# Performance work log

Hardware: AMD Instinct MI355X
Metric: run time of the kernel (lower is better)

The kernel has to match this reference:

```python
import jax, jax.numpy as jnp
import numpy as np

N = 8192
IN_F = 512
OUT_F = 64
ALPHA = 0.2  # LeakyReLU negative slope
NEG_INF = -9e15


def setup_inputs() -> dict:
    key = jax.random.key(0)
    k1, k2, k3, k4 = jax.random.split(key, 4)
    x = jax.random.normal(k1, (N, IN_F), dtype=jnp.float32)
    adj = jax.random.randint(k2, (N, N), 0, 2, dtype=jnp.int32)
    # xavier_uniform with gain=1.414
    def xavier(k, shape, gain=1.414):
        fan_in, fan_out = shape[0], shape[1]
        a = gain * np.sqrt(6.0 / (fan_in + fan_out))
        return jax.random.uniform(k, shape, jnp.float32, -a, a)
    W = xavier(k3, (IN_F, OUT_F))
    a = xavier(k4, (2 * OUT_F, 1))
    return {"x": x, "adj": adj, "W": W, "a": a}


def reference(x, adj, W, a):
    h = x @ W  # [N, F]
    f = W.shape[1]
    # e[i,j] = leakyrelu([h_i, h_j] @ a) = leakyrelu(h_i@a1 + h_j@a2)
    e1 = h @ a[:f, 0]   # [N]
    e2 = h @ a[f:, 0]   # [N]
    e = jax.nn.leaky_relu(e1[:, None] + e2[None, :], negative_slope=ALPHA)  # [N, N]
    scores = jnp.where(adj > 0, e, NEG_INF)
    attention = jax.nn.softmax(scores, axis=1)  # dropout p=0.0 -> identity
    h_prime = attention @ h  # [N, F]
    return jax.nn.elu(h_prime)  # concat=True
```

## Files before the change

### kernel.cpp

```cpp
#include <hip/hip_runtime.h>
#include <hip/hip_bf16.h>

#define NN 8192
#define KF 512
#define FF 64
#define GAT_ALPHA 0.2f
#define MSHIFT 20.0f
#define LOG2E 1.44269504f

#define JSPLIT 16
#define JW (NN / JSPLIT)
#define KSTEPS (JW / 32)

#define HTS 520

#define EXP2F(x) __builtin_amdgcn_exp2f(x)

typedef __attribute__((ext_vector_type(8))) __bf16 bf16x8;
typedef __attribute__((ext_vector_type(4))) float f32x4;

__device__ __forceinline__ unsigned pack_bf16_rne(float hi, float lo) {
    unsigned uh = __float_as_uint(hi);
    unsigned ul = __float_as_uint(lo);
    uh = uh + 0x7FFFu + ((uh >> 16) & 1u);
    ul = ul + 0x7FFFu + ((ul >> 16) & 1u);
    return (uh & 0xFFFF0000u) | (ul >> 16);
}

__global__ __launch_bounds__(256) void gat_linear(
    const float* __restrict__ x, const float* __restrict__ W,
    const float* __restrict__ av, __hip_bfloat16* __restrict__ ht,
    float* __restrict__ e1, float* __restrict__ e2)
{
    __shared__ float xs[32][33];
    __shared__ float Ws[32][64];
    __shared__ float ep[2][32][17];

    const int t  = threadIdx.x;
    const int fq = t & 15;
    const int rq = t >> 4;
    const int i0 = blockIdx.x * 32;

    const int kl = t & 31, r0 = t >> 5;
    const int fw = t & 63, kq = t >> 6;

    float acc[2][4] = {};

    for (int kt = 0; kt < KF; kt += 32) {
        #pragma unroll
        for (int m = 0; m < 4; ++m)
            xs[kl][r0 + 8 * m] = x[(size_t)(i0 + r0 + 8 * m) * KF + kt + kl];
        #pragma unroll
        for (int m = 0; m < 8; ++m)
            Ws[kq + 4 * m][fw] = W[(size_t)(kt + kq + 4 * m) * FF + fw];
        __syncthreads();
        #pragma unroll
        for (int kk = 0; kk < 32; ++kk) {
            float x0 = xs[kk][rq * 2];
            float x1 = xs[kk][rq * 2 + 1];
            f32x4 wv = *(const f32x4*)&Ws[kk][fq * 4];
            #pragma unroll
            for (int v = 0; v < 4; ++v) {
                acc[0][v] += x0 * wv[v];
                acc[1][v] += x1 * wv[v];
            }
        }
        __syncthreads();
    }

    #pragma unroll
    for (int v = 0; v < 4; ++v) {
        int f = fq * 4 + v;
        unsigned w = pack_bf16_rne(acc[1][v], acc[0][v]);
        *(unsigned*)&ht[(size_t)f * NN + i0 + rq * 2] = w;
    }

    f32x4 a1v = *(const f32x4*)&av[fq * 4];
    f32x4 a2v = *(const f32x4*)&av[64 + fq * 4];
    #pragma unroll
    for (int u = 0; u < 2; ++u) {
        float s1 = 0.f, s2 = 0.f;
        #pragma unroll
        for (int v = 0; v < 4; ++v) {
            s1 += acc[u][v] * a1v[v];
            s2 += acc[u][v] * a2v[v];
        }
        ep[0][rq * 2 + u][fq] = s1;
        ep[1][rq * 2 + u][fq] = s2;
    }
    __syncthreads();
    if (t < 32) {
        float s1 = 0.f, s2 = 0.f;
        #pragma unroll
        for (int q = 0; q < 16; ++q) { s1 += ep[0][t][q]; s2 += ep[1][t][q]; }
        e1[i0 + t] = s1 * LOG2E;
        e2[i0 + t] = s2 * LOG2E;
    }
}

__global__ __launch_bounds__(256) void gat_attn(
    const int* __restrict__ adj, const __hip_bfloat16* __restrict__ ht,
    const float* __restrict__ e1, const float* __restrict__ e2,
    float* __restrict__ accs, float* __restrict__ lsums)
{
    __shared__ __hip_bfloat16 hs[64 * HTS];
    __shared__ float e2s[JW];
    __shared__ unsigned char msk[KSTEPS * 4 * 68];

    const int t     = threadIdx.x;
    const int lane  = t & 63;
    const int wv    = t >> 6;
    const int n16   = lane & 15;
    const int quad  = lane >> 4;
    const int split = blockIdx.x & (JSPLIT - 1);
    const int i0b   = (blockIdx.x >> 4) * 64;
    const int i0    = i0b + wv * 16;
    const int j0    = split * JW;
    const int rowl  = wv * 16 + n16;
    const int row   = i0 + n16;

    #pragma unroll
    for (int k = 0; k < 16; ++k) {
        int g  = t + k * 256;
        int f  = g >> 6;
        int jl = (g & 63) * 8;
        *(bf16x8*)&hs[f * HTS + jl] =
            *(const bf16x8*)&ht[(size_t)f * NN + j0 + jl];
    }
    if (t < JW / 4)
        *(float4*)&e2s[t * 4] = *(const float4*)&e2[j0 + t * 4];

    {
        const int st = t & 15;
        #pragma unroll
        for (int rep = 0; rep < 4; ++rep) {
            const int r = rep * 16 + (t >> 4);
            const int* ap = adj + (size_t)(i0b + r) * NN + j0 + st * 32;
            unsigned w = 0;
            #pragma unroll
            for (int k = 0; k < 8; ++k) {
                int4 v = *(const int4*)(ap + k * 4);
                unsigned nib =  (unsigned)(v.x > 0)
                             | ((unsigned)(v.y > 0) << 1)
                             | ((unsigned)(v.z > 0) << 2)
                             | ((unsigned)(v.w > 0) << 3);
                w |= nib << (k * 4);
            }
            msk[(st * 4 + 0) * 68 + r] = (unsigned char)(w       & 0xFF);
            msk[(st * 4 + 1) * 68 + r] = (unsigned char)((w >> 8)  & 0xFF);
            msk[(st * 4 + 2) * 68 + r] = (unsigned char)((w >> 16) & 0xFF);
            msk[(st * 4 + 3) * 68 + r] = (unsigned char)((w >> 24) & 0xFF);
        }
    }
    __syncthreads();

    const float e1L = e1[row];
    float ms = e1L + MSHIFT * LOG2E;
    const float miL = ms > 0.f ? ms : GAT_ALPHA * ms;
    const float c0  = e1L - miL;
    const float c1  = GAT_ALPHA * e1L - miL;

    const __hip_bfloat16* hp = hs + rowl * 0 + n16 * HTS + quad * 8;
    const float* ep0 = e2s + quad * 8;

    f32x4 dacc0 = {0.f,0.f,0.f,0.f}, dacc1 = {0.f,0.f,0.f,0.f};
    f32x4 dacc2 = {0.f,0.f,0.f,0.f}, dacc3 = {0.f,0.f,0.f,0.f};
    f32x4 dl    = {0.f,0.f,0.f,0.f};

    typedef __attribute__((ext_vector_type(4))) int i32x4;
    const i32x4 ones_i = {0x3F803F80, 0x3F803F80, 0x3F803F80, 0x3F803F80};
    const bf16x8 ones  = __builtin_bit_cast(bf16x8, ones_i);

    unsigned mb = msk[(0 * 4 + quad) * 68 + rowl];
    f32x4  e0 = *(const f32x4*)(ep0);
    f32x4  ev = *(const f32x4*)(ep0 + 4);
    bf16x8 b0 = *(const bf16x8*)(hp);
    bf16x8 b1 = *(const bf16x8*)(hp + 16 * HTS);
    bf16x8 b2 = *(const bf16x8*)(hp + 32 * HTS);
    bf16x8 b3 = *(const bf16x8*)(hp + 48 * HTS);

    for (int st = 0; st < KSTEPS; ++st) {
        const unsigned mc = mb;
        const f32x4  ce0 = e0, cev = ev;
        const bf16x8 cb0 = b0, cb1 = b1, cb2 = b2, cb3 = b3;
        if (st + 1 < KSTEPS) {
            mb = msk[((st + 1) * 4 + quad) * 68 + rowl];
            e0 = *(const f32x4*)(ep0 + (st + 1) * 32);
            ev = *(const f32x4*)(ep0 + (st + 1) * 32 + 4);
            b0 = *(const bf16x8*)(hp + (st + 1) * 32);
            b1 = *(const bf16x8*)(hp + 16 * HTS + (st + 1) * 32);
            b2 = *(const bf16x8*)(hp + 32 * HTS + (st + 1) * 32);
            b3 = *(const bf16x8*)(hp + 48 * HTS + (st + 1) * 32);
        }

#define PJ(eval, bit)                                                          \
        ( ((mc >> (bit)) & 1u)                                                 \
            ? EXP2F(fmaxf(c0 + (eval), __builtin_fmaf(GAT_ALPHA, (eval), c1))) \
            : 0.f )
        float p0 = PJ(ce0.x, 0);
        float p1 = PJ(ce0.y, 1);
        float p2 = PJ(ce0.z, 2);
        float p3 = PJ(ce0.w, 3);
        float p4 = PJ(cev.x, 4);
        float p5 = PJ(cev.y, 5);
        float p6 = PJ(cev.z, 6);
        float p7 = PJ(cev.w, 7);
#undef PJ
        i32x4 iv;
        iv.x = (int)pack_bf16_rne(p1, p0);
        iv.y = (int)pack_bf16_rne(p3, p2);
        iv.z = (int)pack_bf16_rne(p5, p4);
        iv.w = (int)pack_bf16_rne(p7, p6);
        bf16x8 af = __builtin_bit_cast(bf16x8, iv);

        dacc0 = __builtin_amdgcn_mfma_f32_16x16x32_bf16(af, cb0, dacc0, 0, 0, 0);
        dacc1 = __builtin_amdgcn_mfma_f32_16x16x32_bf16(af, cb1, dacc1, 0, 0, 0);
        dacc2 = __builtin_amdgcn_mfma_f32_16x16x32_bf16(af, cb2, dacc2, 0, 0, 0);
        dacc3 = __builtin_amdgcn_mfma_f32_16x16x32_bf16(af, cb3, dacc3, 0, 0, 0);
        dl    = __builtin_amdgcn_mfma_f32_16x16x32_bf16(af, ones, dl, 0, 0, 0);
    }

    if (n16 == 0) {
        lsums[(size_t)split * NN + i0 + quad * 4 + 0] = dl.x;
        lsums[(size_t)split * NN + i0 + quad * 4 + 1] = dl.y;
        lsums[(size_t)split * NN + i0 + quad * 4 + 2] = dl.z;
        lsums[(size_t)split * NN + i0 + quad * 4 + 3] = dl.w;
    }

    float* ab = accs + (size_t)split * NN * FF + (size_t)(i0 + quad * 4) * FF + n16;
#define STORE4(dv, ftofs)                                                      \
    ab[0 * FF + (ftofs)] = (dv).x;                                             \
    ab[1 * FF + (ftofs)] = (dv).y;                                             \
    ab[2 * FF + (ftofs)] = (dv).z;                                             \
    ab[3 * FF + (ftofs)] = (dv).w;
    STORE4(dacc0, 0)
    STORE4(dacc1, 16)
    STORE4(dacc2, 32)
    STORE4(dacc3, 48)
#undef STORE4
}

__global__ __launch_bounds__(256) void gat_epilogue(
    const float* __restrict__ accs, const float* __restrict__ lsums,
    float* __restrict__ out)
{
    const int idx = (blockIdx.x * 256 + threadIdx.x) * 4;
    const int row = idx >> 6;

    float l = 0.f;
    #pragma unroll
    for (int s = 0; s < JSPLIT; ++s) l += lsums[(size_t)s * NN + row];

    f32x4 a = {0.f, 0.f, 0.f, 0.f};
    #pragma unroll
    for (int s = 0; s < JSPLIT; ++s) {
        f32x4 v = *(const f32x4*)(accs + (size_t)s * NN * FF + idx);
        a.x += v.x; a.y += v.y; a.z += v.z; a.w += v.w;
    }

    const float li = 1.f / l;
    f32x4 o;
    o.x = a.x * li; o.y = a.y * li; o.z = a.z * li; o.w = a.w * li;
    o.x = o.x > 0.f ? o.x : __expf(o.x) - 1.f;
    o.y = o.y > 0.f ? o.y : __expf(o.y) - 1.f;
    o.z = o.z > 0.f ? o.z : __expf(o.z) - 1.f;
    o.w = o.w > 0.f ? o.w : __expf(o.w) - 1.f;
    *(f32x4*)(out + idx) = o;
}

extern "C" void kernel_launch(void* const* d_in, const int* in_sizes, int n_in,
                              void* d_out, int out_size, void* d_ws, size_t ws_size,
                              hipStream_t stream) {
    const float* x   = (const float*)d_in[0];
    const int*   adj = (const int*)d_in[1];
    const float* W   = (const float*)d_in[2];
    const float* av  = (const float*)d_in[3];
    float* out = (float*)d_out;

    char* wsb = (char*)d_ws;
    __hip_bfloat16* ht = (__hip_bfloat16*)wsb;
    float* e1    = (float*)(wsb + (1 << 20));
    float* e2    = e1 + NN;
    float* accs  = e2 + NN;
    float* lsums = accs + (size_t)JSPLIT * NN * FF;

    gat_linear<<<256, 256, 0, stream>>>(x, W, av, ht, e1, e2);
    gat_attn<<<(NN / 64) * JSPLIT, 256, 0, stream>>>(adj, ht, e1, e2, accs, lsums);
    gat_epilogue<<<NN * FF / 1024, 256, 0, stream>>>(accs, lsums, out);
}
```

Baseline: 399.8 us.

## Stream adjacency and h directly from global memory, dropping LDS staging

Removes the shared-memory staging of the h tile, e2 slice and packed adjacency bitmask in the attention kernel. Each lane now reads its adjacency ints, e2 values and h fragments straight from global memory, with adjacency prefetched two steps ahead and the rest one step ahead. A minBlocks occupancy hint of 4 is added to launch_bounds. This drops the block-wide prologue and barrier and frees LDS to allow more resident blocks, but h and e2 reuse now depends on L2/L1 caching, and per-lane adjacency loads are less coalesced than the previous cooperative load.

```diff
diff --git a/kernel.cpp b/kernel.cpp
--- a/kernel.cpp
+++ b/kernel.cpp
@@ -12,12 +12,11 @@
 #define JW (NN / JSPLIT)
 #define KSTEPS (JW / 32)
 
-#define HTS 520
-
 #define EXP2F(x) __builtin_amdgcn_exp2f(x)
 
 typedef __attribute__((ext_vector_type(8))) __bf16 bf16x8;
 typedef __attribute__((ext_vector_type(4))) float f32x4;
+typedef __attribute__((ext_vector_type(4))) int i32x4;
 
 __device__ __forceinline__ unsigned pack_bf16_rne(float hi, float lo) {
     unsigned uh = __float_as_uint(hi);
@@ -98,61 +97,20 @@
     }
 }
 
-__global__ __launch_bounds__(256) void gat_attn(
+__global__ __launch_bounds__(256, 4) void gat_attn(
     const int* __restrict__ adj, const __hip_bfloat16* __restrict__ ht,
     const float* __restrict__ e1, const float* __restrict__ e2,
     float* __restrict__ accs, float* __restrict__ lsums)
 {
-    __shared__ __hip_bfloat16 hs[64 * HTS];
-    __shared__ float e2s[JW];
-    __shared__ unsigned char msk[KSTEPS * 4 * 68];
-
     const int t     = threadIdx.x;
     const int lane  = t & 63;
     const int wv    = t >> 6;
     const int n16   = lane & 15;
     const int quad  = lane >> 4;
     const int split = blockIdx.x & (JSPLIT - 1);
-    const int i0b   = (blockIdx.x >> 4) * 64;
-    const int i0    = i0b + wv * 16;
+    const int i0    = (blockIdx.x >> 4) * 64 + wv * 16;
     const int j0    = split * JW;
-    const int rowl  = wv * 16 + n16;
     const int row   = i0 + n16;
-
-    #pragma unroll
-    for (int k = 0; k < 16; ++k) {
-        int g  = t + k * 256;
-        int f  = g >> 6;
-        int jl = (g & 63) * 8;
-        *(bf16x8*)&hs[f * HTS + jl] =
-            *(const bf16x8*)&ht[(size_t)f * NN + j0 + jl];
-    }
-    if (t < JW / 4)
-        *(float4*)&e2s[t * 4] = *(const float4*)&e2[j0 + t * 4];
-
-    {
-        const int st = t & 15;
-        #pragma unroll
-        for (int rep = 0; rep < 4; ++rep) {
-            const int r = rep * 16 + (t >> 4);
-            const int* ap = adj + (size_t)(i0b + r) * NN + j0 + st * 32;
-            unsigned w = 0;
-            #pragma unroll
-            for (int k = 0; k < 8; ++k) {
-                int4 v = *(const int4*)(ap + k * 4);
-                unsigned nib =  (unsigned)(v.x > 0)
-                             | ((unsigned)(v.y > 0) << 1)
-                             | ((unsigned)(v.z > 0) << 2)
-                             | ((unsigned)(v.w > 0) << 3);
-                w |= nib << (k * 4);
-            }
-            msk[(st * 4 + 0) * 68 + r] = (unsigned char)(w       & 0xFF);
-            msk[(st * 4 + 1) * 68 + r] = (unsigned char)((w >> 8)  & 0xFF);
-            msk[(st * 4 + 2) * 68 + r] = (unsigned char)((w >> 16) & 0xFF);
-            msk[(st * 4 + 3) * 68 + r] = (unsigned char)((w >> 24) & 0xFF);
-        }
-    }
-    __syncthreads();
 
     const float e1L = e1[row];
     float ms = e1L + MSHIFT * LOG2E;
@@ -160,51 +118,61 @@
     const float c0  = e1L - miL;
     const float c1  = GAT_ALPHA * e1L - miL;
 
-    const __hip_bfloat16* hp = hs + rowl * 0 + n16 * HTS + quad * 8;
-    const float* ep0 = e2s + quad * 8;
+    const int jb = j0 + quad * 8;
+    const int*            __restrict__ ap  = adj + (size_t)row * NN + jb;
+    const float*          __restrict__ e2p = e2 + jb;
+    const __hip_bfloat16* __restrict__ hb  = ht + (size_t)n16 * NN + jb;
 
     f32x4 dacc0 = {0.f,0.f,0.f,0.f}, dacc1 = {0.f,0.f,0.f,0.f};
     f32x4 dacc2 = {0.f,0.f,0.f,0.f}, dacc3 = {0.f,0.f,0.f,0.f};
     f32x4 dl    = {0.f,0.f,0.f,0.f};
 
-    typedef __attribute__((ext_vector_type(4))) int i32x4;
     const i32x4 ones_i = {0x3F803F80, 0x3F803F80, 0x3F803F80, 0x3F803F80};
     const bf16x8 ones  = __builtin_bit_cast(bf16x8, ones_i);
 
-    unsigned mb = msk[(0 * 4 + quad) * 68 + rowl];
-    f32x4  e0 = *(const f32x4*)(ep0);
-    f32x4  ev = *(const f32x4*)(ep0 + 4);
-    bf16x8 b0 = *(const bf16x8*)(hp);
-    bf16x8 b1 = *(const bf16x8*)(hp + 16 * HTS);
-    bf16x8 b2 = *(const bf16x8*)(hp + 32 * HTS);
-    bf16x8 b3 = *(const bf16x8*)(hp + 48 * HTS);
+    i32x4 aN0 = *(const i32x4*)(ap);
+    i32x4 aN1 = *(const i32x4*)(ap + 4);
+    i32x4 aM0 = *(const i32x4*)(ap + 32);
+    i32x4 aM1 = *(const i32x4*)(ap + 36);
+    f32x4  e0 = *(const f32x4*)(e2p);
+    f32x4  ev = *(const f32x4*)(e2p + 4);
+    bf16x8 b0 = *(const bf16x8*)(hb);
+    bf16x8 b1 = *(const bf16x8*)(hb + (size_t)16 * NN);
+    bf16x8 b2 = *(const bf16x8*)(hb + (size_t)32 * NN);
+    bf16x8 b3 = *(const bf16x8*)(hb + (size_t)48 * NN);
 
     for (int st = 0; st < KSTEPS; ++st) {
-        const unsigned mc = mb;
-        const f32x4  ce0 = e0, cev = ev;
+        const i32x4  ca0 = aN0, ca1 = aN1;
+        const f32x4  ce0 = e0,  cev = ev;
         const bf16x8 cb0 = b0, cb1 = b1, cb2 = b2, cb3 = b3;
+        aN0 = aM0; aN1 = aM1;
+        if (st + 2 < KSTEPS) {
+            const int o = (st + 2) * 32;
+            aM0 = *(const i32x4*)(ap + o);
+            aM1 = *(const i32x4*)(ap + o + 4);
+        }
         if (st + 1 < KSTEPS) {
-            mb = msk[((st + 1) * 4 + quad) * 68 + rowl];
-            e0 = *(const f32x4*)(ep0 + (st + 1) * 32);
-            ev = *(const f32x4*)(ep0 + (st + 1) * 32 + 4);
-            b0 = *(const bf16x8*)(hp + (st + 1) * 32);
-            b1 = *(const bf16x8*)(hp + 16 * HTS + (st + 1) * 32);
-            b2 = *(const bf16x8*)(hp + 32 * HTS + (st + 1) * 32);
-            b3 = *(const bf16x8*)(hp + 48 * HTS + (st + 1) * 32);
-        }
-
-#define PJ(eval, bit)                                                          \
-        ( ((mc >> (bit)) & 1u)                                                 \
+            const int o = (st + 1) * 32;
+            e0 = *(const f32x4*)(e2p + o);
+            ev = *(const f32x4*)(e2p + o + 4);
+            b0 = *(const bf16x8*)(hb + o);
+            b1 = *(const bf16x8*)(hb + (size_t)16 * NN + o);
+            b2 = *(const bf16x8*)(hb + (size_t)32 * NN + o);
+            b3 = *(const bf16x8*)(hb + (size_t)48 * NN + o);
+        }
+
+#define PJ(eval, an)                                                           \
+        ( (an) > 0                                                             \
             ? EXP2F(fmaxf(c0 + (eval), __builtin_fmaf(GAT_ALPHA, (eval), c1))) \
             : 0.f )
-        float p0 = PJ(ce0.x, 0);
-        float p1 = PJ(ce0.y, 1);
-        float p2 = PJ(ce0.z, 2);
-        float p3 = PJ(ce0.w, 3);
-        float p4 = PJ(cev.x, 4);
-        float p5 = PJ(cev.y, 5);
-        float p6 = PJ(cev.z, 6);
-        float p7 = PJ(cev.w, 7);
+        float p0 = PJ(ce0.x, ca0.x);
+        float p1 = PJ(ce0.y, ca0.y);
+        float p2 = PJ(ce0.z, ca0.z);
+        float p3 = PJ(ce0.w, ca0.w);
+        float p4 = PJ(cev.x, ca1.x);
+        float p5 = PJ(cev.y, ca1.y);
+        float p6 = PJ(cev.z, ca1.z);
+        float p7 = PJ(cev.w, ca1.w);
 #undef PJ
         i32x4 iv;
         iv.x = (int)pack_bf16_rne(p1, p0);
```

Result: slower. 429.0 us (+7.3%).

## Stream adjacency directly into registers with double-buffered prefetch in attention kernel

Applied to the files above, without the earlier changes.

Drops the shared-memory bitmask staging of the adjacency matrix. Each lane now loads its own adj row slice straight into registers, double-buffered across four groups of steps and overlapped with the exp/MFMA work, and the K loop is fully unrolled. It also sets launch_bounds(256,2) to target two blocks per CU. The aim is to hide the 256MB adjacency read behind compute and remove the prologue stall and LDS mask traffic. In exchange, register pressure rises (64 extra VGPRs for the buffers), and the per-lane global loads are less coalesced: each lane reads 2×16B chunks from separate rows.

```diff
diff --git a/kernel.cpp b/kernel.cpp
--- a/kernel.cpp
+++ b/kernel.cpp
@@ -9,6 +9,7 @@
 #define LOG2E 1.44269504f
 
 #define JSPLIT 16
+#define JSHIFT 4
 #define JW (NN / JSPLIT)
 #define KSTEPS (JW / 32)
 
@@ -18,6 +19,7 @@
 
 typedef __attribute__((ext_vector_type(8))) __bf16 bf16x8;
 typedef __attribute__((ext_vector_type(4))) float f32x4;
+typedef __attribute__((ext_vector_type(4))) int i32x4;
 
 __device__ __forceinline__ unsigned pack_bf16_rne(float hi, float lo) {
     unsigned uh = __float_as_uint(hi);
@@ -98,14 +100,13 @@
     }
 }
 
-__global__ __launch_bounds__(256) void gat_attn(
+__global__ __launch_bounds__(256, 2) void gat_attn(
     const int* __restrict__ adj, const __hip_bfloat16* __restrict__ ht,
     const float* __restrict__ e1, const float* __restrict__ e2,
     float* __restrict__ accs, float* __restrict__ lsums)
 {
     __shared__ __hip_bfloat16 hs[64 * HTS];
     __shared__ float e2s[JW];
-    __shared__ unsigned char msk[KSTEPS * 4 * 68];
 
     const int t     = threadIdx.x;
     const int lane  = t & 63;
@@ -113,10 +114,8 @@
     const int n16   = lane & 15;
     const int quad  = lane >> 4;
     const int split = blockIdx.x & (JSPLIT - 1);
-    const int i0b   = (blockIdx.x >> 4) * 64;
-    const int i0    = i0b + wv * 16;
+    const int i0    = (blockIdx.x >> JSHIFT) * 64 + wv * 16;
     const int j0    = split * JW;
-    const int rowl  = wv * 16 + n16;
     const int row   = i0 + n16;
 
     #pragma unroll
@@ -130,28 +129,22 @@
     if (t < JW / 4)
         *(float4*)&e2s[t * 4] = *(const float4*)&e2[j0 + t * 4];
 
-    {
-        const int st = t & 15;
-        #pragma unroll
-        for (int rep = 0; rep < 4; ++rep) {
-            const int r = rep * 16 + (t >> 4);
-            const int* ap = adj + (size_t)(i0b + r) * NN + j0 + st * 32;
-            unsigned w = 0;
-            #pragma unroll
-            for (int k = 0; k < 8; ++k) {
-                int4 v = *(const int4*)(ap + k * 4);
-                unsigned nib =  (unsigned)(v.x > 0)
-                             | ((unsigned)(v.y > 0) << 1)
-                             | ((unsigned)(v.z > 0) << 2)
-                             | ((unsigned)(v.w > 0) << 3);
-                w |= nib << (k * 4);
-            }
-            msk[(st * 4 + 0) * 68 + r] = (unsigned char)(w       & 0xFF);
-            msk[(st * 4 + 1) * 68 + r] = (unsigned char)((w >> 8)  & 0xFF);
-            msk[(st * 4 + 2) * 68 + r] = (unsigned char)((w >> 16) & 0xFF);
-            msk[(st * 4 + 3) * 68 + r] = (unsigned char)((w >> 24) & 0xFF);
-        }
-    }
+    const int* __restrict__ apL = adj + (size_t)row * NN + j0 + quad * 8;
+    i32x4 bufA[8], bufB[8];
+
+#define ISSUE(BUF, stb)                                                        \
+    BUF[0] = *(const i32x4*)(apL + (stb) * 128 + 0);                           \
+    BUF[1] = *(const i32x4*)(apL + (stb) * 128 + 4);                           \
+    BUF[2] = *(const i32x4*)(apL + (stb) * 128 + 32);                          \
+    BUF[3] = *(const i32x4*)(apL + (stb) * 128 + 36);                          \
+    BUF[4] = *(const i32x4*)(apL + (stb) * 128 + 64);                          \
+    BUF[5] = *(const i32x4*)(apL + (stb) * 128 + 68);                          \
+    BUF[6] = *(const i32x4*)(apL + (stb) * 128 + 96);                          \
+    BUF[7] = *(const i32x4*)(apL + (stb) * 128 + 100);
+
+    ISSUE(bufA, 0)
+    ISSUE(bufB, 1)
+
     __syncthreads();
 
     const float e1L = e1[row];
@@ -160,18 +153,16 @@
     const float c0  = e1L - miL;
     const float c1  = GAT_ALPHA * e1L - miL;
 
-    const __hip_bfloat16* hp = hs + rowl * 0 + n16 * HTS + quad * 8;
+    const __hip_bfloat16* hp = hs + n16 * HTS + quad * 8;
     const float* ep0 = e2s + quad * 8;
 
     f32x4 dacc0 = {0.f,0.f,0.f,0.f}, dacc1 = {0.f,0.f,0.f,0.f};
     f32x4 dacc2 = {0.f,0.f,0.f,0.f}, dacc3 = {0.f,0.f,0.f,0.f};
     f32x4 dl    = {0.f,0.f,0.f,0.f};
 
-    typedef __attribute__((ext_vector_type(4))) int i32x4;
     const i32x4 ones_i = {0x3F803F80, 0x3F803F80, 0x3F803F80, 0x3F803F80};
     const bf16x8 ones  = __builtin_bit_cast(bf16x8, ones_i);
 
-    unsigned mb = msk[(0 * 4 + quad) * 68 + rowl];
     f32x4  e0 = *(const f32x4*)(ep0);
     f32x4  ev = *(const f32x4*)(ep0 + 4);
     bf16x8 b0 = *(const bf16x8*)(hp);
@@ -179,46 +170,66 @@
     bf16x8 b2 = *(const bf16x8*)(hp + 32 * HTS);
     bf16x8 b3 = *(const bf16x8*)(hp + 48 * HTS);
 
-    for (int st = 0; st < KSTEPS; ++st) {
-        const unsigned mc = mb;
-        const f32x4  ce0 = e0, cev = ev;
-        const bf16x8 cb0 = b0, cb1 = b1, cb2 = b2, cb3 = b3;
-        if (st + 1 < KSTEPS) {
-            mb = msk[((st + 1) * 4 + quad) * 68 + rowl];
-            e0 = *(const f32x4*)(ep0 + (st + 1) * 32);
-            ev = *(const f32x4*)(ep0 + (st + 1) * 32 + 4);
-            b0 = *(const bf16x8*)(hp + (st + 1) * 32);
-            b1 = *(const bf16x8*)(hp + 16 * HTS + (st + 1) * 32);
-            b2 = *(const bf16x8*)(hp + 32 * HTS + (st + 1) * 32);
-            b3 = *(const bf16x8*)(hp + 48 * HTS + (st + 1) * 32);
-        }
-
-#define PJ(eval, bit)                                                          \
-        ( ((mc >> (bit)) & 1u)                                                 \
+#define PJ(eval, an)                                                           \
+        ( (an) > 0                                                             \
             ? EXP2F(fmaxf(c0 + (eval), __builtin_fmaf(GAT_ALPHA, (eval), c1))) \
             : 0.f )
-        float p0 = PJ(ce0.x, 0);
-        float p1 = PJ(ce0.y, 1);
-        float p2 = PJ(ce0.z, 2);
-        float p3 = PJ(ce0.w, 3);
-        float p4 = PJ(cev.x, 4);
-        float p5 = PJ(cev.y, 5);
-        float p6 = PJ(cev.z, 6);
-        float p7 = PJ(cev.w, 7);
+
+#define STEP(stg, AX0, AX1)                                                    \
+    {                                                                          \
+        const f32x4  ce0 = e0, cev = ev;                                       \
+        const bf16x8 cb0 = b0, cb1 = b1, cb2 = b2, cb3 = b3;                   \
+        if ((stg) + 1 < KSTEPS) {                                              \
+            e0 = *(const f32x4*)(ep0 + ((stg) + 1) * 32);                      \
+            ev = *(const f32x4*)(ep0 + ((stg) + 1) * 32 + 4);                  \
+            b0 = *(const bf16x8*)(hp + ((stg) + 1) * 32);                      \
+            b1 = *(const bf16x8*)(hp + 16 * HTS + ((stg) + 1) * 32);           \
+            b2 = *(const bf16x8*)(hp + 32 * HTS + ((stg) + 1) * 32);           \
+            b3 = *(const bf16x8*)(hp + 48 * HTS + ((stg) + 1) * 32);           \
+        }                                                                      \
+        float p0 = PJ(ce0.x, (AX0).x);                                         \
+        float p1 = PJ(ce0.y, (AX0).y);                                         \
+        float p2 = PJ(ce0.z, (AX0).z);                                         \
+        float p3 = PJ(ce0.w, (AX0).w);                                         \
+        float p4 = PJ(cev.x, (AX1).x);                                         \
+        float p5 = PJ(cev.y, (AX1).y);                                         \
+        float p6 = PJ(cev.z, (AX1).z);                                         \
+        float p7 = PJ(cev.w, (AX1).w);                                         \
+        i32x4 iv;                                                              \
+        iv.x = (int)pack_bf16_rne(p1, p0);                                     \
+        iv.y = (int)pack_bf16_rne(p3, p2);                                     \
+        iv.z = (int)pack_bf16_rne(p5, p4);                                     \
+        iv.w = (int)pack_bf16_rne(p7, p6);                                     \
+        bf16x8 af = __builtin_bit_cast(bf16x8, iv);                            \
+        dacc0 = __builtin_amdgcn_mfma_f32_16x16x32_bf16(af, cb0, dacc0, 0,0,0);\
+        dacc1 = __builtin_amdgcn_mfma_f32_16x16x32_bf16(af, cb1, dacc1, 0,0,0);\
+        dacc2 = __builtin_amdgcn_mfma_f32_16x16x32_bf16(af, cb2, dacc2, 0,0,0);\
+        dacc3 = __builtin_amdgcn_mfma_f32_16x16x32_bf16(af, cb3, dacc3, 0,0,0);\
+        dl    = __builtin_amdgcn_mfma_f32_16x16x32_bf16(af, ones, dl,   0,0,0);\
+    }
+
+    STEP( 0, bufA[0], bufA[1])
+    STEP( 1, bufA[2], bufA[3])
+    STEP( 2, bufA[4], bufA[5])
+    STEP( 3, bufA[6], bufA[7])
+    ISSUE(bufA, 2)
+    STEP( 4, bufB[0], bufB[1])
+    STEP( 5, bufB[2], bufB[3])
+    STEP( 6, bufB[4], bufB[5])
+    STEP( 7, bufB[6], bufB[7])
+    ISSUE(bufB, 3)
+    STEP( 8, bufA[0], bufA[1])
+    STEP( 9, bufA[2], bufA[3])
+    STEP(10, bufA[4], bufA[5])
+    STEP(11, bufA[6], bufA[7])
+    STEP(12, bufB[0], bufB[1])
+    STEP(13, bufB[2], bufB[3])
+    STEP(14, bufB[4], bufB[5])
+    STEP(15, bufB[6], bufB[7])
+
+#undef STEP
 #undef PJ
-        i32x4 iv;
-        iv.x = (int)pack_bf16_rne(p1, p0);
-        iv.y = (int)pack_bf16_rne(p3, p2);
-        iv.z = (int)pack_bf16_rne(p5, p4);
-        iv.w = (int)pack_bf16_rne(p7, p6);
-        bf16x8 af = __builtin_bit_cast(bf16x8, iv);
-
-        dacc0 = __builtin_amdgcn_mfma_f32_16x16x32_bf16(af, cb0, dacc0, 0, 0, 0);
-        dacc1 = __builtin_amdgcn_mfma_f32_16x16x32_bf16(af, cb1, dacc1, 0, 0, 0);
-        dacc2 = __builtin_amdgcn_mfma_f32_16x16x32_bf16(af, cb2, dacc2, 0, 0, 0);
-        dacc3 = __builtin_amdgcn_mfma_f32_16x16x32_bf16(af, cb3, dacc3, 0, 0, 0);
-        dl    = __builtin_amdgcn_mfma_f32_16x16x32_bf16(af, ones, dl, 0, 0, 0);
-    }
+#undef ISSUE
 
     if (n16 == 0) {
         lsums[(size_t)split * NN + i0 + quad * 4 + 0] = dl.x;
```

New measurement: 400.0 us. About the same (+0.0%).
